# Optimization experiments

Measured on AMD Instinct MI355X. Metric: run time of the kernel, lower is better.

Reference implementation:

```python
import jax, jax.numpy as jnp
import numpy as np

N = 100000
E = 1600000
D = 256

def setup_inputs() -> dict:
    key = jax.random.key(0)
    k1, k2, k3 = jax.random.split(key, 3)
    nodes = jax.random.normal(k1, (N, D), dtype=jnp.float32)
    edge_index = jax.random.randint(k2, (2, E), 0, N, dtype=jnp.int64)
    W = jax.random.normal(k3, (D, D), dtype=jnp.float32) * 0.05  # GCN lin weight [out,in]
    b = jnp.zeros((D,), dtype=jnp.float32)
    gamma = jnp.ones((D,), dtype=jnp.float32)
    beta = jnp.zeros((D,), dtype=jnp.float32)
    return {"nodes": nodes, "edge_index": edge_index, "W": W, "b": b,
            "gamma": gamma, "beta": beta}

def reference(nodes, edge_index, W, b, gamma, beta):
    n = nodes.shape[0]
    loop = jnp.arange(n, dtype=edge_index.dtype)
    src = jnp.concatenate([edge_index[0], loop])  # add self-loops (PyG default)
    dst = jnp.concatenate([edge_index[1], loop])
    # linear transform
    x = nodes @ W.T  # [N, D]
    # symmetric normalization: deg from target index, weight 1 per edge
    deg = jnp.zeros((n,), dtype=x.dtype).at[dst].add(1.0)
    dinv = jnp.where(deg > 0, jax.lax.rsqrt(deg), 0.0)
    norm = dinv[src] * dinv[dst]  # [E+N]
    msg = x[src] * norm[:, None]
    out = jax.ops.segment_sum(msg, dst, num_segments=n) + b  # [N, D]
    # LayerNorm over feature dim
    mu = jnp.mean(out, axis=-1, keepdims=True)
    var = jnp.mean(jnp.square(out - mu), axis=-1, keepdims=True)
    out = (out - mu) * jax.lax.rsqrt(var + 1e-5) * gamma + beta
    # ReLU; dropout is identity in eval mode
    return jax.nn.relu(out)
```

## Files before the change

kernel.cpp:

```cpp
#include <hip/hip_runtime.h>
#include <hip/hip_bf16.h>

#define NN 100000
#define EE 1600000
#define DD 256
#define CAP 48
#define NPART 391
#define ABLK 800
#define ACHUNK 2000

typedef __bf16 bf16x8 __attribute__((ext_vector_type(8)));
typedef float f32x4 __attribute__((ext_vector_type(4)));
typedef float f32x2 __attribute__((ext_vector_type(2)));

__device__ __forceinline__ unsigned short f2bf(float f) {
    unsigned u = __builtin_bit_cast(unsigned, f);
    u += 0x7fffu + ((u >> 16) & 1u);
    return (unsigned short)(u >> 16);
}
__device__ __forceinline__ float bf2f(unsigned short h) {
    unsigned u = ((unsigned)h) << 16;
    return __builtin_bit_cast(float, u);
}
__device__ __forceinline__ unsigned cvtpk(float a, float b) {
    unsigned r;
    asm("v_cvt_pk_bf16_f32 %0, %1, %2" : "=v"(r) : "v"(a), "v"(b));
    return r;
}

__global__ __launch_bounds__(256) void k_partA(const void* __restrict__ eptr,
        unsigned int* __restrict__ gseg2, int* __restrict__ cnts, int* __restrict__ pref) {
    __shared__ int lcnt[NPART];
    __shared__ int lcnt2[NPART];
    __shared__ int lpref[NPART];
    __shared__ int sA[512], sB[512];
    __shared__ __align__(16) unsigned int stash[ACHUNK];
    __shared__ unsigned short stashp[ACHUNK];
    __shared__ __align__(16) unsigned int sorted[ACHUNK];
    __shared__ int lflag;
    const int b = blockIdx.x, tid = threadIdx.x;
    if (tid == 0) lflag = 0;
    for (int i = tid; i < NPART; i += 256) { lcnt[i] = 0; lcnt2[i] = 0; }
    __syncthreads();
    if (tid < 64) {
        const unsigned long long w = ((const unsigned long long*)eptr)[tid];
        if (w > 0xFFFFFFFFULL) lflag = 1;
    }
    __syncthreads();
    const int is32 = lflag;
    const int e0 = b * ACHUNK;
    for (int e = e0 + tid; e < e0 + ACHUNK; e += 256) {
        int ss, dd;
        if (is32) { const int* p = (const int*)eptr; ss = p[e]; dd = p[EE + e]; }
        else { const long long* p = (const long long*)eptr; ss = (int)p[e]; dd = (int)p[EE + e]; }
        const int li = e - e0;
        stash[li]  = ((unsigned)ss << 8) | (unsigned)(dd & 255);
        stashp[li] = (unsigned short)(dd >> 8);
        atomicAdd(&lcnt[dd >> 8], 1);
    }
    __syncthreads();
    sA[tid]       = (tid < NPART) ? lcnt[tid] : 0;
    sA[tid + 256] = (tid + 256 < NPART) ? lcnt[tid + 256] : 0;
    __syncthreads();
    int* s = sA; int* d2 = sB;
    for (int off = 1; off < 512; off <<= 1) {
        d2[tid]       = s[tid]       + (tid >= off ? s[tid - off] : 0);
        d2[tid + 256] = s[tid + 256] + (tid + 256 >= off ? s[tid + 256 - off] : 0);
        __syncthreads();
        int* t = s; s = d2; d2 = t;
    }
    for (int i = tid; i < NPART; i += 256) {
        lpref[i] = (i == 0) ? 0 : s[i - 1];
        cnts[(size_t)i * ABLK + b] = lcnt[i];
        pref[(size_t)i * ABLK + b] = (i == 0) ? 0 : s[i - 1];
    }
    __syncthreads();
    for (int li = tid; li < ACHUNK; li += 256) {
        const unsigned int w = stash[li];
        const int pp = stashp[li];
        const int slot = atomicAdd(&lcnt2[pp], 1);
        sorted[lpref[pp] + slot] = w;
    }
    __syncthreads();
    for (int li4 = tid; li4 < ACHUNK / 4; li4 += 256)
        *(uint4*)(gseg2 + (size_t)b * ACHUNK + (size_t)li4 * 4) = *(const uint4*)&sorted[li4 * 4];
}

__global__ __launch_bounds__(256) void k_partB(const unsigned int* __restrict__ gseg2,
        const int* __restrict__ cnts, const int* __restrict__ pref,
        int* __restrict__ bucket, int* __restrict__ cnt) {
    __shared__ int lc[256];
    __shared__ __align__(16) int lb[256 * CAP];
    const int p = blockIdx.x, tid = threadIdx.x;
    const int node0 = p * 256 + tid;
    lc[tid] = 1;
    lb[tid * CAP] = node0;
    __syncthreads();
    for (int bb = tid; bb < ABLK; bb += 256) {
        const int c = cnts[(size_t)p * ABLK + bb];
        const unsigned int* seg = gseg2 + (size_t)bb * ACHUNK + pref[(size_t)p * ABLK + bb];
        for (int i = 0; i < c; ++i) {
            const unsigned int en = seg[i];
            const int d = en & 255;
            const int slot = atomicAdd(&lc[d], 1);
            if (slot < CAP) lb[d * CAP + slot] = (int)(en >> 8);
        }
    }
    __syncthreads();
    const size_t base = (size_t)p * 256 * CAP;
    #pragma unroll
    for (int it = 0; it < CAP / 4; ++it) {
        const int idx4 = it * 256 + tid;
        const int node = p * 256 + idx4 / (CAP / 4);
        if (node < NN)
            *(uint4*)(bucket + base + (size_t)idx4 * 4) = *(const uint4*)&lb[idx4 * 4];
    }
    if (node0 < NN) cnt[node0] = lc[tid];
}

__global__ void k_detect(const unsigned long long* __restrict__ e64, int* __restrict__ flag) {
    if (threadIdx.x == 0 && blockIdx.x == 0) {
        int is32 = 0;
        for (int i = 0; i < 64; ++i)
            if (e64[i] > 0xFFFFFFFFULL) is32 = 1;
        *flag = is32;
    }
}
__global__ __launch_bounds__(256) void k_init(int* __restrict__ cnt, int* __restrict__ bucket) {
    int v = blockIdx.x * 256 + threadIdx.x;
    if (v < NN) { cnt[v] = 1; bucket[(size_t)v * CAP] = v; }
}
__global__ __launch_bounds__(256) void k_count_scatter(const void* __restrict__ eptr,
        const int* __restrict__ flag, int* __restrict__ cnt, int* __restrict__ bucket) {
    int e = blockIdx.x * 256 + threadIdx.x;
    if (e >= EE) return;
    int s, d;
    if (*flag) { const int* p = (const int*)eptr; s = p[e]; d = p[EE + e]; }
    else { const long long* p = (const long long*)eptr; s = (int)p[e]; d = (int)p[EE + e]; }
    int slot = atomicAdd(&cnt[d], 1);
    if (slot < CAP) bucket[(size_t)d * CAP + slot] = s;
}

__global__ __launch_bounds__(256) void k_wconv(const float* __restrict__ W,
        unsigned short* __restrict__ wf) {
    const int s = blockIdx.x * 256 + threadIdx.x;
    const int lane = s & 63;
    const int ks = (s >> 6) & 7;
    const int g  = (s >> 9) & 3;
    const int wv = s >> 11;
    const int feat = wv * 64 + g * 16 + (lane & 15);
    const int k0 = ks * 32 + (lane >> 4) * 8;
    const float* wp = W + (size_t)feat * 256 + k0;
    unsigned short o[8];
    #pragma unroll
    for (int j = 0; j < 8; ++j) o[j] = f2bf(wp[j]);
    uint4 pk;
    pk.x = o[0] | ((unsigned)o[1] << 16); pk.y = o[2] | ((unsigned)o[3] << 16);
    pk.z = o[4] | ((unsigned)o[5] << 16); pk.w = o[6] | ((unsigned)o[7] << 16);
    *(uint4*)(wf + (size_t)s * 8) = pk;
}

__global__ __launch_bounds__(256) void k_gemm(const float* __restrict__ nodes,
        const unsigned short* __restrict__ wf, const int* __restrict__ cnt,
        unsigned short* __restrict__ y) {
    __shared__ __align__(16) unsigned short xlds[64][264];
    const int tid = threadIdx.x, lane = tid & 63, wv = tid >> 6;
    const int q = lane >> 4, n0 = lane & 15;

    const int row0 = blockIdx.x * 64;
    #pragma unroll
    for (int rr = 0; rr < 16; ++rr) {
        const int idx = rr * 256 + tid;
        const int r = idx >> 6, c4 = idx & 63;
        const int grow = min(row0 + r, NN - 1);
        const float4 v = *(const float4*)(nodes + (size_t)grow * 256 + c4 * 4);
        uint2 pk;
        pk.x = cvtpk(v.x, v.y);
        pk.y = cvtpk(v.z, v.w);
        *(uint2*)&xlds[r][c4 * 4] = pk;
    }
    __syncthreads();

    f32x4 acc[4][4];
    #pragma unroll
    for (int sub = 0; sub < 4; ++sub)
        #pragma unroll
        for (int g = 0; g < 4; ++g) acc[sub][g] = (f32x4){0, 0, 0, 0};

    #pragma unroll
    for (int ks = 0; ks < 8; ++ks) {
        bf16x8 a[4];
        #pragma unroll
        for (int g = 0; g < 4; ++g)
            a[g] = *(const bf16x8*)(wf + ((((size_t)wv * 4 + g) * 8 + ks) * 64 + lane) * 8);
        #pragma unroll
        for (int sub = 0; sub < 4; ++sub) {
            const bf16x8 xf = *(const bf16x8*)&xlds[sub * 16 + n0][ks * 32 + q * 8];
            #pragma unroll
            for (int g = 0; g < 4; ++g)
                acc[sub][g] = __builtin_amdgcn_mfma_f32_16x16x32_bf16(a[g], xf, acc[sub][g], 0, 0, 0);
        }
    }

    #pragma unroll
    for (int sub = 0; sub < 4; ++sub) {
        const int node = row0 + sub * 16 + n0;
        if (node < NN) {
            const float dval = rsqrtf((float)cnt[node]);
            unsigned short* yp = y + (size_t)node * 256 + wv * 64 + q * 4;
            #pragma unroll
            for (int g = 0; g < 4; ++g) {
                const float e0 = acc[sub][g][0] * dval, e1 = acc[sub][g][1] * dval;
                const float e2 = acc[sub][g][2] * dval, e3 = acc[sub][g][3] * dval;
                uint2 pk;
                pk.x = cvtpk(e0, e1);
                pk.y = cvtpk(e2, e3);
                *(uint2*)(yp + g * 16) = pk;
            }
        }
    }
}

__global__ __launch_bounds__(256) void k_gather(const unsigned short* __restrict__ y,
        const int* __restrict__ cnt, const int* __restrict__ bucket,
        const float* __restrict__ bias, const float* __restrict__ gamma,
        const float* __restrict__ beta, float* __restrict__ out) {
    const int v = blockIdx.x * 4 + (threadIdx.x >> 6);
    const int lane = threadIdx.x & 63;
    const int h = lane >> 5, l = lane & 31;
    const int c = cnt[v];
    const int my = bucket[(size_t)v * CAP + lane];
    const int m = min(c, CAP);

    f32x2 a2[4] = {{0,0},{0,0},{0,0},{0,0}};
    #define ACCUM(P) do {                                                      \
        a2[0] += (f32x2){__builtin_bit_cast(float, (P).x << 16),               \
                         __builtin_bit_cast(float, (P).x & 0xffff0000u)};      \
        a2[1] += (f32x2){__builtin_bit_cast(float, (P).y << 16),               \
                         __builtin_bit_cast(float, (P).y & 0xffff0000u)};      \
        a2[2] += (f32x2){__builtin_bit_cast(float, (P).z << 16),               \
                         __builtin_bit_cast(float, (P).z & 0xffff0000u)};      \
        a2[3] += (f32x2){__builtin_bit_cast(float, (P).w << 16),               \
                         __builtin_bit_cast(float, (P).w & 0xffff0000u)};      \
    } while (0)

    int j = 0;
    uint4 P0 = {0,0,0,0}, P1 = {0,0,0,0}, P2 = {0,0,0,0}, P3 = {0,0,0,0};
    const bool have8 = (m >= 8);
    if (have8) {
        const int s0 = __shfl(my, 0 + h), s1 = __shfl(my, 2 + h);
        const int s2 = __shfl(my, 4 + h), s3 = __shfl(my, 6 + h);
        P0 = *((const uint4*)(y + (size_t)s0 * 256) + l);
        P1 = *((const uint4*)(y + (size_t)s1 * 256) + l);
        P2 = *((const uint4*)(y + (size_t)s2 * 256) + l);
        P3 = *((const uint4*)(y + (size_t)s3 * 256) + l);
    }
    for (; j + 16 <= m; j += 8) {
        const int s0 = __shfl(my, j + 8 + h),  s1 = __shfl(my, j + 10 + h);
        const int s2 = __shfl(my, j + 12 + h), s3 = __shfl(my, j + 14 + h);
        const uint4 q0 = *((const uint4*)(y + (size_t)s0 * 256) + l);
        const uint4 q1 = *((const uint4*)(y + (size_t)s1 * 256) + l);
        const uint4 q2 = *((const uint4*)(y + (size_t)s2 * 256) + l);
        const uint4 q3 = *((const uint4*)(y + (size_t)s3 * 256) + l);
        ACCUM(P0); ACCUM(P1); ACCUM(P2); ACCUM(P3);
        P0 = q0; P1 = q1; P2 = q2; P3 = q3;
    }
    if (have8) {
        ACCUM(P0); ACCUM(P1); ACCUM(P2); ACCUM(P3);
        j += 8;
    }
    for (; j + 4 <= m; j += 4) {
        const int s0 = __shfl(my, j + h);
        const int s1 = __shfl(my, j + 2 + h);
        const uint4 p0 = *((const uint4*)(y + (size_t)s0 * 256) + l);
        const uint4 p1 = *((const uint4*)(y + (size_t)s1 * 256) + l);
        ACCUM(p0); ACCUM(p1);
    }
    for (; j + 2 <= m; j += 2) {
        const int s0 = __shfl(my, j + h);
        const uint4 p0 = *((const uint4*)(y + (size_t)s0 * 256) + l);
        ACCUM(p0);
    }
    if (j < m) {
        const int st = __shfl(my, j);
        if (h == 0) {
            const uint4 p0 = *((const uint4*)(y + (size_t)st * 256) + l);
            ACCUM(p0);
        }
    }
    #undef ACCUM

    float acc[8];
    acc[0] = a2[0].x; acc[1] = a2[0].y; acc[2] = a2[1].x; acc[3] = a2[1].y;
    acc[4] = a2[2].x; acc[5] = a2[2].y; acc[6] = a2[3].x; acc[7] = a2[3].y;

    #pragma unroll
    for (int i = 0; i < 8; ++i) acc[i] += __shfl_xor(acc[i], 32);

    const float dvv = rsqrtf((float)c);
    const float4 b0 = *(const float4*)(bias + l * 8);
    const float4 b1 = *(const float4*)(bias + l * 8 + 4);
    float u[8];
    u[0] = acc[0] * dvv + b0.x; u[1] = acc[1] * dvv + b0.y;
    u[2] = acc[2] * dvv + b0.z; u[3] = acc[3] * dvv + b0.w;
    u[4] = acc[4] * dvv + b1.x; u[5] = acc[5] * dvv + b1.y;
    u[6] = acc[6] * dvv + b1.z; u[7] = acc[7] * dvv + b1.w;

    float s1 = 0, s2 = 0;
    #pragma unroll
    for (int i = 0; i < 8; ++i) { s1 += u[i]; s2 += u[i] * u[i]; }
    #pragma unroll
    for (int o = 16; o > 0; o >>= 1) {
        s1 += __shfl_xor(s1, o);
        s2 += __shfl_xor(s2, o);
    }
    const float mean = s1 * (1.0f / 256.0f);
    const float var  = s2 * (1.0f / 256.0f) - mean * mean;
    const float rstd = rsqrtf(var + 1e-5f);

    const float4 g0 = *(const float4*)(gamma + l * 8);
    const float4 g1 = *(const float4*)(gamma + l * 8 + 4);
    const float4 e0 = *(const float4*)(beta + l * 8);
    const float4 e1 = *(const float4*)(beta + l * 8 + 4);
    float o8[8];
    o8[0] = fmaxf(0.0f, (u[0] - mean) * rstd * g0.x + e0.x);
    o8[1] = fmaxf(0.0f, (u[1] - mean) * rstd * g0.y + e0.y);
    o8[2] = fmaxf(0.0f, (u[2] - mean) * rstd * g0.z + e0.z);
    o8[3] = fmaxf(0.0f, (u[3] - mean) * rstd * g0.w + e0.w);
    o8[4] = fmaxf(0.0f, (u[4] - mean) * rstd * g1.x + e1.x);
    o8[5] = fmaxf(0.0f, (u[5] - mean) * rstd * g1.y + e1.y);
    o8[6] = fmaxf(0.0f, (u[6] - mean) * rstd * g1.z + e1.z);
    o8[7] = fmaxf(0.0f, (u[7] - mean) * rstd * g1.w + e1.w);
    float4 ov;
    if (h == 0) { ov.x = o8[0]; ov.y = o8[1]; ov.z = o8[2]; ov.w = o8[3]; }
    else        { ov.x = o8[4]; ov.y = o8[5]; ov.z = o8[6]; ov.w = o8[7]; }
    *(float4*)(out + (size_t)v * 256 + l * 8 + h * 4) = ov;
}

extern "C" void kernel_launch(void* const* d_in, const int* in_sizes, int n_in,
                              void* d_out, int out_size, void* d_ws, size_t ws_size,
                              hipStream_t stream) {
    const float* nodes = (const float*)d_in[0];
    const void*  edges = d_in[1];
    const float* W     = (const float*)d_in[2];
    const float* b     = (const float*)d_in[3];
    const float* gamma = (const float*)d_in[4];
    const float* beta  = (const float*)d_in[5];
    float* out = (float*)d_out;

    char* ws = (char*)d_ws;
    size_t off = 0;
    auto alloc = [&](size_t bytes) { size_t p = off; off = (off + bytes + 255) & ~(size_t)255; return p; };
    int*            cnt    = (int*)(ws + alloc((size_t)NN * 4));
    int*            flag   = (int*)(ws + alloc(256));
    int*            bucket = (int*)(ws + alloc((size_t)NN * CAP * 4));
    unsigned short* y      = (unsigned short*)(ws + alloc((size_t)NN * DD * 2));
    unsigned short* wf     = (unsigned short*)(ws + alloc((size_t)DD * DD * 2));
    int*            cnts   = (int*)(ws + alloc((size_t)NPART * ABLK * 4));
    int*            pref   = (int*)(ws + alloc((size_t)NPART * ABLK * 4));
    unsigned int*   gseg2  = (unsigned int*)(ws + alloc((size_t)EE * 4));
    const size_t full_need = off;
    (void)in_sizes; (void)n_in; (void)out_size;

    k_wconv<<<32, 256, 0, stream>>>(W, wf);
    if (ws_size >= full_need) {
        k_partA<<<ABLK, 256, 0, stream>>>(edges, gseg2, cnts, pref);
        k_partB<<<NPART, 256, 0, stream>>>(gseg2, cnts, pref, bucket, cnt);
    } else {
        k_detect<<<1, 64, 0, stream>>>((const unsigned long long*)edges, flag);
        k_init<<<(NN + 255) / 256, 256, 0, stream>>>(cnt, bucket);
        k_count_scatter<<<(EE + 255) / 256, 256, 0, stream>>>(edges, flag, cnt, bucket);
    }
    k_gemm<<<(NN + 63) / 64, 256, 0, stream>>>(nodes, wf, cnt, y);
    k_gather<<<NN / 4, 256, 0, stream>>>(y, cnt, bucket, b, gamma, beta, out);
}
```

Baseline: 374.7 us.

## Fuse weight conversion into partition kernel, widen partB blocks, split gather launches

Moves the W-to-bf16 conversion into the first 32 blocks of the edge-partition kernel, which removes a separate launch. The bucket-building kernel now uses 512 threads per block, so per-partition segment scanning is spread over more threads. The gather kernel is split into four launches over node quarters, likely as a scheduling or timing experiment. Four gather launches add launch overhead in exchange for any tail or cache effect.

```diff
diff --git a/kernel.cpp b/kernel.cpp
--- a/kernel.cpp
+++ b/kernel.cpp
@@ -8,6 +8,7 @@
 #define NPART 391
 #define ABLK 800
 #define ACHUNK 2000
+#define GQ 25000
 
 typedef __bf16 bf16x8 __attribute__((ext_vector_type(8)));
 typedef float f32x4 __attribute__((ext_vector_type(4)));
@@ -29,7 +30,8 @@
 }
 
 __global__ __launch_bounds__(256) void k_partA(const void* __restrict__ eptr,
-        unsigned int* __restrict__ gseg2, int* __restrict__ cnts, int* __restrict__ pref) {
+        unsigned int* __restrict__ gseg2, int* __restrict__ cnts, int* __restrict__ pref,
+        const float* __restrict__ W, unsigned short* __restrict__ wf) {
     __shared__ int lcnt[NPART];
     __shared__ int lcnt2[NPART];
     __shared__ int lpref[NPART];
@@ -84,19 +86,38 @@
     __syncthreads();
     for (int li4 = tid; li4 < ACHUNK / 4; li4 += 256)
         *(uint4*)(gseg2 + (size_t)b * ACHUNK + (size_t)li4 * 4) = *(const uint4*)&sorted[li4 * 4];
-}
-
-__global__ __launch_bounds__(256) void k_partB(const unsigned int* __restrict__ gseg2,
+
+    if (b < 32) {
+        const int sl = b * 256 + tid;
+        const int lane = sl & 63;
+        const int ks = (sl >> 6) & 7;
+        const int g  = (sl >> 9) & 3;
+        const int wv = sl >> 11;
+        const int feat = wv * 64 + g * 16 + (lane & 15);
+        const int k0 = ks * 32 + (lane >> 4) * 8;
+        const float* wp = W + (size_t)feat * 256 + k0;
+        unsigned short o[8];
+        #pragma unroll
+        for (int j = 0; j < 8; ++j) o[j] = f2bf(wp[j]);
+        uint4 pk;
+        pk.x = o[0] | ((unsigned)o[1] << 16); pk.y = o[2] | ((unsigned)o[3] << 16);
+        pk.z = o[4] | ((unsigned)o[5] << 16); pk.w = o[6] | ((unsigned)o[7] << 16);
+        *(uint4*)(wf + (size_t)sl * 8) = pk;
+    }
+}
+
+__global__ __launch_bounds__(512) void k_partB(const unsigned int* __restrict__ gseg2,
         const int* __restrict__ cnts, const int* __restrict__ pref,
         int* __restrict__ bucket, int* __restrict__ cnt) {
     __shared__ int lc[256];
     __shared__ __align__(16) int lb[256 * CAP];
     const int p = blockIdx.x, tid = threadIdx.x;
-    const int node0 = p * 256 + tid;
-    lc[tid] = 1;
-    lb[tid * CAP] = node0;
-    __syncthreads();
-    for (int bb = tid; bb < ABLK; bb += 256) {
+    if (tid < 256) {
+        lc[tid] = 1;
+        lb[tid * CAP] = p * 256 + tid;
+    }
+    __syncthreads();
+    for (int bb = tid; bb < ABLK; bb += 512) {
         const int c = cnts[(size_t)p * ABLK + bb];
         const unsigned int* seg = gseg2 + (size_t)bb * ACHUNK + pref[(size_t)p * ABLK + bb];
         for (int i = 0; i < c; ++i) {
@@ -109,13 +130,13 @@
     __syncthreads();
     const size_t base = (size_t)p * 256 * CAP;
     #pragma unroll
-    for (int it = 0; it < CAP / 4; ++it) {
-        const int idx4 = it * 256 + tid;
+    for (int it = 0; it < (256 * CAP / 4) / 512; ++it) {
+        const int idx4 = it * 512 + tid;
         const int node = p * 256 + idx4 / (CAP / 4);
         if (node < NN)
             *(uint4*)(bucket + base + (size_t)idx4 * 4) = *(const uint4*)&lb[idx4 * 4];
     }
-    if (node0 < NN) cnt[node0] = lc[tid];
+    if (tid < 256 && p * 256 + tid < NN) cnt[p * 256 + tid] = lc[tid];
 }
 
 __global__ void k_detect(const unsigned long long* __restrict__ e64, int* __restrict__ flag) {
@@ -224,8 +245,8 @@
 __global__ __launch_bounds__(256) void k_gather(const unsigned short* __restrict__ y,
         const int* __restrict__ cnt, const int* __restrict__ bucket,
         const float* __restrict__ bias, const float* __restrict__ gamma,
-        const float* __restrict__ beta, float* __restrict__ out) {
-    const int v = blockIdx.x * 4 + (threadIdx.x >> 6);
+        const float* __restrict__ beta, float* __restrict__ out, int vbase) {
+    const int v = vbase + blockIdx.x * 4 + (threadIdx.x >> 6);
     const int lane = threadIdx.x & 63;
     const int h = lane >> 5, l = lane & 31;
     const int c = cnt[v];
@@ -362,15 +383,18 @@
     const size_t full_need = off;
     (void)in_sizes; (void)n_in; (void)out_size;
 
-    k_wconv<<<32, 256, 0, stream>>>(W, wf);
     if (ws_size >= full_need) {
-        k_partA<<<ABLK, 256, 0, stream>>>(edges, gseg2, cnts, pref);
-        k_partB<<<NPART, 256, 0, stream>>>(gseg2, cnts, pref, bucket, cnt);
+        k_partA<<<ABLK, 256, 0, stream>>>(edges, gseg2, cnts, pref, W, wf);
+        k_partB<<<NPART, 512, 0, stream>>>(gseg2, cnts, pref, bucket, cnt);
     } else {
+        k_wconv<<<32, 256, 0, stream>>>(W, wf);
         k_detect<<<1, 64, 0, stream>>>((const unsigned long long*)edges, flag);
         k_init<<<(NN + 255) / 256, 256, 0, stream>>>(cnt, bucket);
         k_count_scatter<<<(EE + 255) / 256, 256, 0, stream>>>(edges, flag, cnt, bucket);
     }
     k_gemm<<<(NN + 63) / 64, 256, 0, stream>>>(nodes, wf, cnt, y);
-    k_gather<<<NN / 4, 256, 0, stream>>>(y, cnt, bucket, b, gamma, beta, out);
-}
+    k_gather<<<GQ / 4, 256, 0, stream>>>(y, cnt, bucket, b, gamma, beta, out, 0);
+    k_gather<<<GQ / 4, 256, 0, stream>>>(y, cnt, bucket, b, gamma, beta, out, GQ);
+    k_gather<<<GQ / 4, 256, 0, stream>>>(y, cnt, bucket, b, gamma, beta, out, 2 * GQ);
+    k_gather<<<GQ / 4, 256, 0, stream>>>(y, cnt, bucket, b, gamma, beta, out, 3 * GQ);
+}
```

Measured after the change: 376.4 us. No clear change (+0.4%).
